# Kernel tuning notes

Measured on AMD Instinct MI355X. Metric: run time of the kernel, lower is better.

## Reference

```python
import jax, jax.numpy as jnp
import numpy as np

B, S, D, H, DFF = 2, 2048, 1024, 16, 4096
DK = D // H
EPS = 1e-05


def setup_inputs() -> dict:
    key = jax.random.key(0)
    ks = jax.random.split(key, 10)
    s = 0.02
    return {
        "x": jax.random.normal(ks[0], (B, S, D), jnp.float32),
        "src_mask": jnp.ones((B, 1, 1, S), jnp.int32),
        "wq": jax.random.normal(ks[1], (D, D), jnp.float32) * s,
        "wk": jax.random.normal(ks[2], (D, D), jnp.float32) * s,
        "wv": jax.random.normal(ks[3], (D, D), jnp.float32) * s,
        "wo": jax.random.normal(ks[4], (D, D), jnp.float32) * s,
        "w1": jax.random.normal(ks[5], (D, DFF), jnp.float32) * s,
        "b1": jnp.zeros((DFF,), jnp.float32),
        "w2": jax.random.normal(ks[6], (DFF, D), jnp.float32) * s,
        "b2": jnp.zeros((D,), jnp.float32),
        "gamma1": jnp.ones((), jnp.float32),
        "beta1": jnp.ones((), jnp.float32),
        "gamma2": jnp.ones((), jnp.float32),
        "beta2": jnp.ones((), jnp.float32),
    }


def layer_norm(x, gamma, beta):
    # torch.var uses unbiased estimator (ddof=1); gamma/beta are scalars
    mean = jnp.mean(x, axis=-1, keepdims=True)
    var = jnp.var(x, axis=-1, keepdims=True, ddof=1)
    return (x - mean) * gamma / jnp.sqrt(var + EPS) + beta


def mha(x, wq, wk, wv, wo):
    # Note: source's masked_fill is non-in-place with discarded result -> mask has no effect.
    q = (x @ wq).reshape(B, S, H, DK).transpose(0, 2, 1, 3)
    k = (x @ wk).reshape(B, S, H, DK).transpose(0, 2, 1, 3)
    v = (x @ wv).reshape(B, S, H, DK).transpose(0, 2, 1, 3)
    scores = jnp.einsum('bhqd,bhkd->bhqk', q, k) / jnp.sqrt(jnp.float32(DK))
    attn = jax.nn.softmax(scores, axis=-1)
    out = jnp.einsum('bhqk,bhkd->bhqd', attn, v)
    out = out.transpose(0, 2, 1, 3).reshape(B, S, D)
    return out @ wo


def reference(x, src_mask, wq, wk, wv, wo, w1, b1, w2, b2,
              gamma1, beta1, gamma2, beta2):
    # residual 1: attention (dropout = identity in eval)
    x = layer_norm(x + mha(x, wq, wk, wv, wo), gamma1, beta1)
    # residual 2: FFN
    ff = jax.nn.relu(x @ w1 + b1) @ w2 + b2
    x = layer_norm(x + ff, gamma2, beta2)
    return x
```

## Files before the change

### kernel.cpp

```cpp
#include <hip/hip_runtime.h>
#include <cstdio>

constexpr int B_   = 2;
constexpr int S_   = 2048;
constexpr int D_   = 1024;
constexpr int H_   = 16;
constexpr int DFF_ = 4096;
constexpr int DK_  = D_ / H_;
constexpr int M_   = B_ * S_;
constexpr float EPS_ = 1e-5f;
constexpr size_t MEGE = 1u << 20;
constexpr size_t QKV_STRIDE = 4 * MEGE;

typedef __attribute__((ext_vector_type(8))) short bf16x8;
typedef __attribute__((ext_vector_type(4))) float f32x4;

__device__ __forceinline__ float bf2f(unsigned int u) {
    return __uint_as_float(u << 16);
}
__device__ __forceinline__ unsigned short f2bf(float f) {
    unsigned int u = __float_as_uint(f);
    unsigned int r = u + 0x7fffu + ((u >> 16) & 1u);
    return (unsigned short)(r >> 16);
}
__device__ __forceinline__ unsigned short f2bf_rz(float f) {
    return (unsigned short)(__float_as_uint(f) >> 16);
}

__device__ __forceinline__ void gload_lds16(const unsigned short* g, unsigned short* l) {
    __builtin_amdgcn_global_load_lds(
        (const __attribute__((address_space(1))) unsigned int*)g,
        (__attribute__((address_space(3))) unsigned int*)l, 16, 0, 0);
}

__device__ __forceinline__ void tr32(const float* __restrict__ W, unsigned short* __restrict__ Wt,
                                     int K, int N, int bx, int by, float* t )
{
    const int tx = threadIdx.x & 31, ty = threadIdx.x >> 5;
    const int n0 = bx * 32, k0 = by * 32;
    #pragma unroll
    for (int p = 0; p < 4; ++p)
        t[(ty + p * 8) * 33 + tx] = W[(size_t)(k0 + ty + p * 8) * N + n0 + tx];
    __syncthreads();
    #pragma unroll
    for (int p = 0; p < 4; ++p)
        Wt[(size_t)(n0 + ty + p * 8) * K + k0 + tx] = f2bf(t[tx * 33 + ty + p * 8]);
}

__global__ __launch_bounds__(256)
void prep_k(const float* __restrict__ wq, const float* __restrict__ wk,
            const float* __restrict__ wv, const float* __restrict__ wo,
            const float* __restrict__ w1, const float* __restrict__ w2,
            const float* __restrict__ x,
            unsigned short* __restrict__ wqt, unsigned short* __restrict__ wkt,
            unsigned short* __restrict__ wvt, unsigned short* __restrict__ wot,
            unsigned short* __restrict__ w1t, unsigned short* __restrict__ w2t,
            unsigned short* __restrict__ xb)
{
    __shared__ float t[32 * 33];
    const int bid = blockIdx.x;
    if (bid < 4096) {
        const int z = bid >> 10, rem = bid & 1023;
        const float* W = (z == 0) ? wq : (z == 1) ? wk : (z == 2) ? wv : wo;
        unsigned short* Wt = (z == 0) ? wqt : (z == 1) ? wkt : (z == 2) ? wvt : wot;
        tr32(W, Wt, D_, D_, rem & 31, rem >> 5, t);
    } else if (bid < 8192) {
        const int rem = bid - 4096;
        tr32(w1, w1t, D_, DFF_, rem & 127, rem >> 7, t);
    } else if (bid < 12288) {
        const int rem = bid - 8192;
        tr32(w2, w2t, DFF_, D_, rem & 31, rem >> 5, t);
    } else {
        const int i = (bid - 12288) * 256 + threadIdx.x;
        float4 f = reinterpret_cast<const float4*>(x)[i];
        ushort4 u;
        u.x = f2bf(f.x); u.y = f2bf(f.y); u.z = f2bf(f.z); u.w = f2bf(f.w);
        reinterpret_cast<ushort4*>(xb)[i] = u;
    }
}

template<int BM, int OMODE, bool RELU>
__global__ __launch_bounds__(512, 2)
void mg2_k(const unsigned short* __restrict__ A,
           const unsigned short* __restrict__ Bt,
           const float* __restrict__ bias,
           unsigned short* __restrict__ C,
           int M, int N, int K, int Kld)
{
    constexpr int MI  = BM / 64;
    constexpr int AMH = (BM == 128) ? 2 : 1;
    __shared__ __align__(16) unsigned short As[2][BM * 64];
    __shared__ __align__(16) unsigned short Bs[2][256 * 64];

    const int z = blockIdx.z;
    A  += (size_t)z * K;
    Bt += (size_t)z * K;
    C  += (size_t)z * ((size_t)M * N);

    const int tid  = threadIdx.x;
    const int w    = tid >> 6, lane = tid & 63;
    const int l15  = lane & 15, quad = lane >> 4;
    const int wm   = w >> 2, wn = w & 3;
    const int m0   = blockIdx.y * BM, n0 = blockIdx.x * 256;
    const int NT   = K >> 6;

    const int srow = lane >> 3;
    const int schk = (lane & 7) ^ srow;
    const int rsw  = l15 & 7;

    f32x4 acc[2][MI][2][2];
    #pragma unroll
    for (int mh = 0; mh < 2; ++mh)
        #pragma unroll
        for (int mi = 0; mi < MI; ++mi)
            #pragma unroll
            for (int nh = 0; nh < 2; ++nh)
                #pragma unroll
                for (int nj = 0; nj < 2; ++nj)
                    acc[mh][mi][nh][nj] = (f32x4){0.f, 0.f, 0.f, 0.f};

    bf16x8 aA[AMH][MI][2];
    bf16x8 b0[2][2], b1[2][2];

    auto stage = [&](int tile, int type) {
        if (tile >= NT) return;
        const int buf = tile & 1;
        unsigned short* dst; const unsigned short* src; int r0;
        if (BM == 256) {
            if      (type == 0) { dst = &As[buf][0];        src = A;  r0 = m0; }
            else if (type == 1) { dst = &Bs[buf][0];        src = Bt; r0 = n0; }
            else if (type == 2) { dst = &Bs[buf][128 * 64]; src = Bt; r0 = n0 + 128; }
            else                { dst = &As[buf][128 * 64]; src = A;  r0 = m0 + 128; }
        } else {
            if      (type == 0) { dst = &Bs[buf][0];        src = Bt; r0 = n0; }
            else if (type == 1) { dst = &As[buf][0];        src = A;  r0 = m0; }
            else                { dst = &Bs[buf][128 * 64]; src = Bt; r0 = n0 + 128; }
        }
        const int k0 = tile * 64;
        #pragma unroll
        for (int g = 0; g < 2; ++g) {
            const int r = w * 16 + g * 8 + srow;
            gload_lds16(src + (size_t)(r0 + r) * Kld + k0 + schk * 8,
                        dst + (w * 16 + g * 8) * 64);
        }
    };
    auto rdA = [&](int buf, int mh, int amh) {
        const unsigned short* base = &As[buf][(BM == 256 && mh) ? 128 * 64 : 0];
        #pragma unroll
        for (int mi = 0; mi < MI; ++mi) {
            const int row = (BM == 256) ? (wm * 64 + mi * 16 + l15)
                                        : (wm * 64 + mh * 32 + mi * 16 + l15);
            const unsigned short* rp = base + row * 64;
            aA[amh][mi][0] = *reinterpret_cast<const bf16x8*>(rp + ((quad    ) ^ rsw) * 8);
            aA[amh][mi][1] = *reinterpret_cast<const bf16x8*>(rp + ((quad + 4) ^ rsw) * 8);
        }
    };
    auto rdB = [&](int buf, int nh, bf16x8 (&b)[2][2]) {
        const unsigned short* base = &Bs[buf][nh ? 128 * 64 : 0];
        #pragma unroll
        for (int nj = 0; nj < 2; ++nj) {
            const int row = wn * 32 + nj * 16 + l15;
            const unsigned short* rp = base + row * 64;
            b[nj][0] = *reinterpret_cast<const bf16x8*>(rp + ((quad    ) ^ rsw) * 8);
            b[nj][1] = *reinterpret_cast<const bf16x8*>(rp + ((quad + 4) ^ rsw) * 8);
        }
    };
    auto mm = [&](int mh, int amh, int nh, bf16x8 (&b)[2][2]) {
        __builtin_amdgcn_s_setprio(1);
        #pragma unroll
        for (int mi = 0; mi < MI; ++mi)
            #pragma unroll
            for (int nj = 0; nj < 2; ++nj) {
                acc[mh][mi][nh][nj] = __builtin_amdgcn_mfma_f32_16x16x32_bf16(
                    aA[amh][mi][0], b[nj][0], acc[mh][mi][nh][nj], 0, 0, 0);
                acc[mh][mi][nh][nj] = __builtin_amdgcn_mfma_f32_16x16x32_bf16(
                    aA[amh][mi][1], b[nj][1], acc[mh][mi][nh][nj], 0, 0, 0);
            }
        __builtin_amdgcn_s_setprio(0);
    };

    if (BM == 256) {
        stage(0, 0); stage(0, 1); stage(0, 2); stage(0, 3);
        stage(1, 0); stage(1, 1); stage(1, 2);
    } else {
        stage(0, 0); stage(0, 1); stage(0, 2);
        stage(1, 0); stage(1, 1);
    }

    for (int t = 0; t < NT; ++t) {
        const int cur = t & 1;
        if (t == NT - 1)    asm volatile("s_waitcnt vmcnt(0)" ::: "memory");
        else if (BM == 256) asm volatile("s_waitcnt vmcnt(6)" ::: "memory");
        else                asm volatile("s_waitcnt vmcnt(4)" ::: "memory");
        __builtin_amdgcn_s_barrier();

        if (BM == 256) {
            rdA(cur, 0, 0); rdB(cur, 0, b0); stage(t + 1, 3);
            __builtin_amdgcn_s_barrier();
            asm volatile("s_waitcnt lgkmcnt(0)" ::: "memory");
            mm(0, 0, 0, b0);
            __builtin_amdgcn_s_barrier();
            rdB(cur, 1, b1); stage(t + 2, 0);
            __builtin_amdgcn_s_barrier();
            asm volatile("s_waitcnt lgkmcnt(0)" ::: "memory");
            mm(0, 0, 1, b1);
            __builtin_amdgcn_s_barrier();
            rdA(cur, 1, 0); stage(t + 2, 1);
            __builtin_amdgcn_s_barrier();
            asm volatile("s_waitcnt lgkmcnt(0)" ::: "memory");
            mm(1, 0, 0, b0);
            __builtin_amdgcn_s_barrier();
            stage(t + 2, 2);
            __builtin_amdgcn_s_barrier();
            asm volatile("s_waitcnt lgkmcnt(0)" ::: "memory");
            mm(1, 0, 1, b1);
        } else {
            rdA(cur, 0, 0); rdA(cur, 1, 1); rdB(cur, 0, b0); stage(t + 1, 2);
            __builtin_amdgcn_s_barrier();
            asm volatile("s_waitcnt lgkmcnt(0)" ::: "memory");
            mm(0, 0, 0, b0); mm(1, 1, 0, b0);
            __builtin_amdgcn_s_barrier();
            rdB(cur, 1, b1); stage(t + 2, 0); stage(t + 2, 1);
            __builtin_amdgcn_s_barrier();
            asm volatile("s_waitcnt lgkmcnt(0)" ::: "memory");
            mm(0, 0, 1, b1); mm(1, 1, 1, b1);
        }
    }

    #pragma unroll
    for (int mh = 0; mh < 2; ++mh)
        #pragma unroll
        for (int mi = 0; mi < MI; ++mi) {
            const int mrow = (BM == 256) ? (mh * 128 + wm * 64 + mi * 16)
                                         : (wm * 64 + mh * 32 + mi * 16);
            #pragma unroll
            for (int r = 0; r < 4; ++r) {
                const int m = m0 + mrow + quad * 4 + r;
                #pragma unroll
                for (int nh = 0; nh < 2; ++nh)
                    #pragma unroll
                    for (int nj = 0; nj < 2; ++nj) {
                        const int n = n0 + nh * 128 + wn * 32 + nj * 16 + l15;
                        float v = acc[mh][mi][nh][nj][r];
                        if (bias) v += bias[n];
                        if (RELU) v = fmaxf(v, 0.0f);
                        size_t o;
                        if (OMODE == 2) {
                            int mat = n >> 10, nn = n & 1023;
                            int b = m >> 11, s = m & 2047;
                            int h = nn >> 6, dk = nn & 63;
                            o = (size_t)mat * QKV_STRIDE + (((size_t)b * H_ + h) * S_ + s) * DK_ + dk;
                        } else {
                            o = (size_t)m * N + n;
                        }
                        C[o] = f2bf(v);
                    }
            }
        }
}

__device__ __forceinline__ float wave_sum(float v) {
    #pragma unroll
    for (int off = 32; off > 0; off >>= 1) v += __shfl_down(v, off, 64);
    return v;
}

constexpr int TQ_ = 128;
constexpr int TK_ = 64;
constexpr int NT_ = S_ / TK_;

__global__ __launch_bounds__(256)
void fattn_k(const unsigned short* __restrict__ Qm, const unsigned short* __restrict__ Km,
             const unsigned short* __restrict__ Vm, unsigned short* __restrict__ O)
{
    const int bh  = blockIdx.x >> 4;
    const int qt  = blockIdx.x & 15;
    const int tid = threadIdx.x;
    const int w = tid >> 6, lane = tid & 63;
    const int quad = lane >> 4, l15 = lane & 15;
    const int sw = l15 & 7;

    __shared__ __align__(16) unsigned short Ks[2][TK_][64];
    __shared__ __align__(16) unsigned short Vt[2][80][64];
    __shared__ __align__(16) unsigned short Ps[4][32][64];

    bf16x8 qf[2][2];
    #pragma unroll
    for (int i = 0; i < 2; ++i) {
        const unsigned short* qp = Qm + ((size_t)bh * S_ + qt * TQ_ + w * 32 + i * 16 + l15) * DK_;
        qf[i][0] = *reinterpret_cast<const bf16x8*>(qp + quad * 8);
        qf[i][1] = *reinterpret_cast<const bf16x8*>(qp + 32 + quad * 8);
    }

    f32x4 o[2][4];
    f32x4 o4[2];
    #pragma unroll
    for (int i = 0; i < 2; ++i) {
        #pragma unroll
        for (int n = 0; n < 4; ++n) o[i][n] = (f32x4){0.f, 0.f, 0.f, 0.f};
        o4[i] = (f32x4){0.f, 0.f, 0.f, 0.f};
    }

    const unsigned short* kg0 = Km + (size_t)bh * S_ * DK_;
    const unsigned short* vg0 = Vm + (size_t)bh * S_ * DK_;
    const int dgrp = tid >> 4;
    const int vkp  = tid & 15;
    const int srow = lane >> 3;
    const int schk = (lane & 7) ^ srow;

    auto stageK = [&](int t, int buf) {
        const unsigned short* src = kg0 + (size_t)t * TK_ * DK_;
        #pragma unroll
        for (int g = 0; g < 2; ++g) {
            const int r0 = w * 16 + g * 8;
            gload_lds16(src + (size_t)(r0 + srow) * DK_ + schk * 8, &Ks[buf][r0][0]);
        }
    };
    auto loadV = [&](int t, ushort4 (&vp)[4]) {
        const unsigned short* vg = vg0 + (size_t)t * TK_ * DK_;
        #pragma unroll
        for (int p = 0; p < 4; ++p)
            vp[p] = reinterpret_cast<const ushort4*>(vg + (size_t)(vkp + p * 16) * DK_)[dgrp];
    };
    auto storeVt = [&](int buf, ushort4 (&vp)[4]) {
        char* base = reinterpret_cast<char*>(&Vt[buf][dgrp * 4][0]);
        const int cs = vkp >> 1, ch = (vkp & 1) << 3;
        ushort4 pk;
        pk.x = vp[0].x; pk.y = vp[1].x; pk.z = vp[2].x; pk.w = vp[3].x;
        *reinterpret_cast<ushort4*>(base + 0 * 128 + (((cs ^ ((dgrp * 4 + 0) & 7)) << 4) + ch)) = pk;
        pk.x = vp[0].y; pk.y = vp[1].y; pk.z = vp[2].y; pk.w = vp[3].y;
        *reinterpret_cast<ushort4*>(base + 1 * 128 + (((cs ^ ((dgrp * 4 + 1) & 7)) << 4) + ch)) = pk;
        pk.x = vp[0].z; pk.y = vp[1].z; pk.z = vp[2].z; pk.w = vp[3].z;
        *reinterpret_cast<ushort4*>(base + 2 * 128 + (((cs ^ ((dgrp * 4 + 2) & 7)) << 4) + ch)) = pk;
        pk.x = vp[0].w; pk.y = vp[1].w; pk.z = vp[2].w; pk.w = vp[3].w;
        *reinterpret_cast<ushort4*>(base + 3 * 128 + (((cs ^ ((dgrp * 4 + 3) & 7)) << 4) + ch)) = pk;
    };

    stageK(0, 0);
    {
        ushort4 vp0[4];
        loadV(0, vp0);
        storeVt(0, vp0);
        for (int idx = tid; idx < 2 * 16 * 64; idx += 256) {
            const int b  = idx >> 10;
            const int rr = (idx >> 6) & 15;
            const int cc = idx & 63;
            Vt[b][64 + rr][((cc >> 3) ^ (rr & 7)) * 8 + (cc & 7)] =
                (rr == 0) ? (unsigned short)0x3F80 : (unsigned short)0;
        }
    }

    for (int t = 0; t < NT_; ++t) {
        const int cur = t & 1, nxt = cur ^ 1;
        __syncthreads();

        const bool hn = (t + 1 < NT_);
        ushort4 vp[4];
        if (hn) { stageK(t + 1, nxt); loadV(t + 1, vp); }

        f32x4 s[2][4];
        __builtin_amdgcn_s_setprio(1);
        #pragma unroll
        for (int n = 0; n < 4; ++n) {
            const unsigned short* kp = &Ks[cur][n * 16 + l15][0];
            bf16x8 b0 = *reinterpret_cast<const bf16x8*>(kp + ((quad ^ sw) << 3));
            bf16x8 b1 = *reinterpret_cast<const bf16x8*>(kp + (((quad + 4) ^ sw) << 3));
            #pragma unroll
            for (int i = 0; i < 2; ++i) {
                f32x4 a2 = (f32x4){0.f, 0.f, 0.f, 0.f};
                a2 = __builtin_amdgcn_mfma_f32_16x16x32_bf16(qf[i][0], b0, a2, 0, 0, 0);
                a2 = __builtin_amdgcn_mfma_f32_16x16x32_bf16(qf[i][1], b1, a2, 0, 0, 0);
                s[i][n] = a2;
            }
        }
        __builtin_amdgcn_s_setprio(0);

        #pragma unroll
        for (int i = 0; i < 2; ++i)
            #pragma unroll
            for (int r = 0; r < 4; ++r) {
                ushort4 pk;
                pk.x = f2bf_rz(__expf(s[i][0][r] * 0.125f));
                pk.y = f2bf_rz(__expf(s[i][1][r] * 0.125f));
                pk.z = f2bf_rz(__expf(s[i][2][r] * 0.125f));
                pk.w = f2bf_rz(__expf(s[i][3][r] * 0.125f));
                const int R = i * 16 + quad * 4 + r;
                *reinterpret_cast<ushort4*>(
                    reinterpret_cast<char*>(&Ps[w][R][0]) +
                    ((((l15 >> 1) ^ (R & 7)) << 4) + ((l15 & 1) << 3))) = pk;
            }

        if (hn) storeVt(nxt, vp);

        bf16x8 pa[2][2];
        #pragma unroll
        for (int i = 0; i < 2; ++i) {
            const unsigned short* pp = &Ps[w][i * 16 + l15][0];
            pa[i][0] = *reinterpret_cast<const bf16x8*>(pp + ((quad ^ sw) << 3));
            pa[i][1] = *reinterpret_cast<const bf16x8*>(pp + (((quad + 4) ^ sw) << 3));
        }
        __builtin_amdgcn_s_setprio(1);
        #pragma unroll
        for (int n = 0; n < 4; ++n) {
            const unsigned short* vb = &Vt[cur][n * 16 + l15][0];
            bf16x8 vb0 = *reinterpret_cast<const bf16x8*>(vb + ((quad ^ sw) << 3));
            bf16x8 vb1 = *reinterpret_cast<const bf16x8*>(vb + (((quad + 4) ^ sw) << 3));
            #pragma unroll
            for (int i = 0; i < 2; ++i) {
                o[i][n] = __builtin_amdgcn_mfma_f32_16x16x32_bf16(pa[i][0], vb0, o[i][n], 0, 0, 0);
                o[i][n] = __builtin_amdgcn_mfma_f32_16x16x32_bf16(pa[i][1], vb1, o[i][n], 0, 0, 0);
            }
        }
        {
            const unsigned short* vb = &Vt[cur][64 + l15][0];
            bf16x8 vb40 = *reinterpret_cast<const bf16x8*>(vb + ((quad ^ sw) << 3));
            bf16x8 vb41 = *reinterpret_cast<const bf16x8*>(vb + (((quad + 4) ^ sw) << 3));
            #pragma unroll
            for (int i = 0; i < 2; ++i) {
                o4[i] = __builtin_amdgcn_mfma_f32_16x16x32_bf16(pa[i][0], vb40, o4[i], 0, 0, 0);
                o4[i] = __builtin_amdgcn_mfma_f32_16x16x32_bf16(pa[i][1], vb41, o4[i], 0, 0, 0);
            }
        }
        __builtin_amdgcn_s_setprio(0);
    }

    const int b = bh >> 4, h = bh & 15;
    #pragma unroll
    for (int i = 0; i < 2; ++i)
        #pragma unroll
        for (int r = 0; r < 4; ++r) {
            float lrv = __shfl(o4[i][r], lane & 0x30, 64);
            float inv = 1.0f / lrv;
            int q = qt * TQ_ + w * 32 + i * 16 + quad * 4 + r;
            unsigned short* op = O + ((size_t)b * S_ + q) * D_ + h * DK_;
            #pragma unroll
            for (int n = 0; n < 4; ++n)
                op[n * 16 + l15] = f2bf(o[i][n][r] * inv);
        }
}

template<bool HAS_BIAS, bool RES_F32, bool OUT_F32>
__global__ __launch_bounds__(256)
void lnr_k(const unsigned short* __restrict__ P0, const unsigned short* __restrict__ P1,
           const void* __restrict__ res, const float* __restrict__ bias,
           const float* __restrict__ gp, const float* __restrict__ bp,
           void* __restrict__ Out)
{
    const int row = blockIdx.x;
    const int tid = threadIdx.x;
    const int lane = tid & 63, wave = tid >> 6;
    __shared__ float rs[4], rss[4];

    const size_t i4 = (size_t)row * 256 + tid;
    const ushort4 a = reinterpret_cast<const ushort4*>(P0)[i4];
    const ushort4 b = reinterpret_cast<const ushort4*>(P1)[i4];
    float v0 = bf2f(a.x) + bf2f(b.x);
    float v1 = bf2f(a.y) + bf2f(b.y);
    float v2 = bf2f(a.z) + bf2f(b.z);
    float v3 = bf2f(a.w) + bf2f(b.w);
    if (RES_F32) {
        float4 rv = reinterpret_cast<const float4*>(res)[i4];
        v0 += rv.x; v1 += rv.y; v2 += rv.z; v3 += rv.w;
    } else {
        ushort4 rv = reinterpret_cast<const ushort4*>(res)[i4];
        v0 += bf2f(rv.x); v1 += bf2f(rv.y); v2 += bf2f(rv.z); v3 += bf2f(rv.w);
    }
    if (HAS_BIAS) {
        float4 bv = reinterpret_cast<const float4*>(bias)[tid];
        v0 += bv.x; v1 += bv.y; v2 += bv.z; v3 += bv.w;
    }

    float s  = v0 + v1 + v2 + v3;
    float ss = v0*v0 + v1*v1 + v2*v2 + v3*v3;
    s = wave_sum(s);
    ss = wave_sum(ss);
    if (lane == 0) { rs[wave] = s; rss[wave] = ss; }
    __syncthreads();
    const float stot  = rs[0] + rs[1] + rs[2] + rs[3];
    const float sstot = rss[0] + rss[1] + rss[2] + rss[3];
    const float mean = stot / (float)D_;
    const float var  = (sstot - (float)D_ * mean * mean) / (float)(D_ - 1);
    const float scl = gp[0] * rsqrtf(var + EPS_);
    const float be = bp[0];

    float o0 = (v0 - mean) * scl + be;
    float o1 = (v1 - mean) * scl + be;
    float o2 = (v2 - mean) * scl + be;
    float o3 = (v3 - mean) * scl + be;
    if (OUT_F32) {
        reinterpret_cast<float4*>(Out)[i4] = make_float4(o0, o1, o2, o3);
    } else {
        ushort4 o;
        o.x = f2bf(o0); o.y = f2bf(o1); o.z = f2bf(o2); o.w = f2bf(o3);
        reinterpret_cast<ushort4*>(Out)[i4] = o;
    }
}

extern "C" void kernel_launch(void* const* d_in, const int* in_sizes, int n_in,
                              void* d_out, int out_size, void* d_ws, size_t ws_size,
                              hipStream_t stream)
{
    const float* x   = (const float*)d_in[0];
    const float* wq  = (const float*)d_in[2];
    const float* wk  = (const float*)d_in[3];
    const float* wv  = (const float*)d_in[4];
    const float* wo  = (const float*)d_in[5];
    const float* w1  = (const float*)d_in[6];
    const float* b1  = (const float*)d_in[7];
    const float* w2  = (const float*)d_in[8];
    const float* b2  = (const float*)d_in[9];
    const float* g1  = (const float*)d_in[10];
    const float* be1 = (const float*)d_in[11];
    const float* g2  = (const float*)d_in[12];
    const float* be2 = (const float*)d_in[13];

    unsigned short* ws = (unsigned short*)d_ws;
    const size_t need_bytes = 32 * MEGE * 2;
    if (ws_size < need_bytes) {
        fprintf(stderr, "kernel_launch: ws too small (%zu < %zu)\n", ws_size, need_bytes);
    }
    unsigned short* wqt = ws + 0 * MEGE;
    unsigned short* wkt = ws + 1 * MEGE;
    unsigned short* wvt = ws + 2 * MEGE;
    unsigned short* wot = ws + 3 * MEGE;
    unsigned short* w1t = ws + 4 * MEGE;
    unsigned short* w2t = ws + 8 * MEGE;
    unsigned short* xb  = ws + 12 * MEGE;
    unsigned short* Q   = ws + 16 * MEGE;
    unsigned short* K   = ws + 20 * MEGE;
    unsigned short* V   = ws + 24 * MEGE;
    unsigned short* AO  = ws + 28 * MEGE;
    unsigned short* x1  = xb;
    unsigned short* WP  = ws + 16 * MEGE;
    unsigned short* h1  = ws + 16 * MEGE;
    unsigned short* FP  = ws + 0 * MEGE;

    prep_k<<<dim3(16384), 256, 0, stream>>>(wq, wk, wv, wo, w1, w2, x,
                                            wqt, wkt, wvt, wot, w1t, w2t, xb);

    mg2_k<256, 2, false><<<dim3(3 * D_ / 256, M_ / 256), 512, 0, stream>>>(
        xb, wqt, nullptr, Q, M_, 3 * D_, D_, D_);

    fattn_k<<<dim3(B_ * H_ * (S_ / TQ_)), 256, 0, stream>>>(Q, K, V, AO);

    mg2_k<128, 0, false><<<dim3(D_ / 256, M_ / 128, 2), 512, 0, stream>>>(
        AO, wot, nullptr, WP, M_, D_, D_ / 2, D_);

    lnr_k<false, true, false><<<dim3(M_), 256, 0, stream>>>(
        WP, WP + 4 * MEGE, x, nullptr, g1, be1, x1);

    mg2_k<256, 0, true><<<dim3(DFF_ / 256, M_ / 256), 512, 0, stream>>>(
        x1, w1t, b1, h1, M_, DFF_, D_, D_);

    mg2_k<128, 0, false><<<dim3(D_ / 256, M_ / 128, 2), 512, 0, stream>>>(
        h1, w2t, nullptr, FP, M_, D_, DFF_ / 2, DFF_);

    lnr_k<true, false, true><<<dim3(M_), 256, 0, stream>>>(
        FP, FP + 4 * MEGE, x1, b2, g2, be2, d_out);
}
```

Baseline: 342.3 us.

## Split attention tile across 8 waves and fold softmax scale into Q projection

The flash-attention kernel now launches 512 threads, so each of eight waves handles 16 query rows instead of 32, and K staging and V loading are divided between the two halves of the block. The 1/sqrt(dk)·log2(e) factor is folded into Q inside the QKV GEMM epilogue, which lets the softmax use a raw v_exp_f32 (exp2) with no per-element multiply. The aim is more waves to hide latency and fewer VALU ops per score. In exchange each wave gets less MFMA reuse per K/V LDS read, and rounding Q after scaling slightly changes numerics.

Measured after the change: 325.7 us. 4.8% less time.

```diff
diff --git a/kernel.cpp b/kernel.cpp
--- a/kernel.cpp
+++ b/kernel.cpp
@@ -11,6 +11,7 @@
 constexpr float EPS_ = 1e-5f;
 constexpr size_t MEGE = 1u << 20;
 constexpr size_t QKV_STRIDE = 4 * MEGE;
+constexpr float QSCALE_ = 0.18033688011112042f;
 
 typedef __attribute__((ext_vector_type(8))) short bf16x8;
 typedef __attribute__((ext_vector_type(4))) float f32x4;
@@ -25,6 +26,11 @@
 }
 __device__ __forceinline__ unsigned short f2bf_rz(float f) {
     return (unsigned short)(__float_as_uint(f) >> 16);
+}
+__device__ __forceinline__ float exp2_fast(float x) {
+    float r;
+    asm("v_exp_f32 %0, %1" : "=v"(r) : "v"(x));
+    return r;
 }
 
 __device__ __forceinline__ void gload_lds16(const unsigned short* g, unsigned short* l) {
@@ -249,6 +255,7 @@
                             int mat = n >> 10, nn = n & 1023;
                             int b = m >> 11, s = m & 2047;
                             int h = nn >> 6, dk = nn & 63;
+                            if (mat == 0) v *= QSCALE_;
                             o = (size_t)mat * QKV_STRIDE + (((size_t)b * H_ + h) * S_ + s) * DK_ + dk;
                         } else {
                             o = (size_t)m * N + n;
@@ -269,7 +276,7 @@
 constexpr int TK_ = 64;
 constexpr int NT_ = S_ / TK_;
 
-__global__ __launch_bounds__(256)
+__global__ __launch_bounds__(512)
 void fattn_k(const unsigned short* __restrict__ Qm, const unsigned short* __restrict__ Km,
              const unsigned short* __restrict__ Vm, unsigned short* __restrict__ O)
 {
@@ -282,24 +289,20 @@
 
     __shared__ __align__(16) unsigned short Ks[2][TK_][64];
     __shared__ __align__(16) unsigned short Vt[2][80][64];
-    __shared__ __align__(16) unsigned short Ps[4][32][64];
-
-    bf16x8 qf[2][2];
-    #pragma unroll
-    for (int i = 0; i < 2; ++i) {
-        const unsigned short* qp = Qm + ((size_t)bh * S_ + qt * TQ_ + w * 32 + i * 16 + l15) * DK_;
-        qf[i][0] = *reinterpret_cast<const bf16x8*>(qp + quad * 8);
-        qf[i][1] = *reinterpret_cast<const bf16x8*>(qp + 32 + quad * 8);
-    }
-
-    f32x4 o[2][4];
-    f32x4 o4[2];
-    #pragma unroll
-    for (int i = 0; i < 2; ++i) {
-        #pragma unroll
-        for (int n = 0; n < 4; ++n) o[i][n] = (f32x4){0.f, 0.f, 0.f, 0.f};
-        o4[i] = (f32x4){0.f, 0.f, 0.f, 0.f};
-    }
+    __shared__ __align__(16) unsigned short Ps[8][16][64];
+
+    bf16x8 qf0, qf1;
+    {
+        const unsigned short* qp = Qm + ((size_t)bh * S_ + qt * TQ_ + w * 16 + l15) * DK_;
+        qf0 = *reinterpret_cast<const bf16x8*>(qp + quad * 8);
+        qf1 = *reinterpret_cast<const bf16x8*>(qp + 32 + quad * 8);
+    }
+
+    f32x4 o[4];
+    f32x4 o4;
+    #pragma unroll
+    for (int n = 0; n < 4; ++n) o[n] = (f32x4){0.f, 0.f, 0.f, 0.f};
+    o4 = (f32x4){0.f, 0.f, 0.f, 0.f};
 
     const unsigned short* kg0 = Km + (size_t)bh * S_ * DK_;
     const unsigned short* vg0 = Vm + (size_t)bh * S_ * DK_;
@@ -310,9 +313,10 @@
 
     auto stageK = [&](int t, int buf) {
         const unsigned short* src = kg0 + (size_t)t * TK_ * DK_;
+        const int wk = w - 4;
         #pragma unroll
         for (int g = 0; g < 2; ++g) {
-            const int r0 = w * 16 + g * 8;
+            const int r0 = wk * 16 + g * 8;
             gload_lds16(src + (size_t)(r0 + srow) * DK_ + schk * 8, &Ks[buf][r0][0]);
         }
     };
@@ -336,18 +340,18 @@
         *reinterpret_cast<ushort4*>(base + 3 * 128 + (((cs ^ ((dgrp * 4 + 3) & 7)) << 4) + ch)) = pk;
     };
 
-    stageK(0, 0);
-    {
+    if (w >= 4) stageK(0, 0);
+    else {
         ushort4 vp0[4];
         loadV(0, vp0);
         storeVt(0, vp0);
-        for (int idx = tid; idx < 2 * 16 * 64; idx += 256) {
-            const int b  = idx >> 10;
-            const int rr = (idx >> 6) & 15;
-            const int cc = idx & 63;
-            Vt[b][64 + rr][((cc >> 3) ^ (rr & 7)) * 8 + (cc & 7)] =
-                (rr == 0) ? (unsigned short)0x3F80 : (unsigned short)0;
-        }
+    }
+    for (int idx = tid; idx < 2 * 16 * 64; idx += 512) {
+        const int b  = idx >> 10;
+        const int rr = (idx >> 6) & 15;
+        const int cc = idx & 63;
+        Vt[b][64 + rr][((cc >> 3) ^ (rr & 7)) * 8 + (cc & 7)] =
+            (rr == 0) ? (unsigned short)0x3F80 : (unsigned short)0;
     }
 
     for (int t = 0; t < NT_; ++t) {
@@ -356,48 +360,42 @@
 
         const bool hn = (t + 1 < NT_);
         ushort4 vp[4];
-        if (hn) { stageK(t + 1, nxt); loadV(t + 1, vp); }
-
-        f32x4 s[2][4];
+        if (hn) { if (w >= 4) stageK(t + 1, nxt); else loadV(t + 1, vp); }
+
+        f32x4 s[4];
         __builtin_amdgcn_s_setprio(1);
         #pragma unroll
         for (int n = 0; n < 4; ++n) {
             const unsigned short* kp = &Ks[cur][n * 16 + l15][0];
             bf16x8 b0 = *reinterpret_cast<const bf16x8*>(kp + ((quad ^ sw) << 3));
             bf16x8 b1 = *reinterpret_cast<const bf16x8*>(kp + (((quad + 4) ^ sw) << 3));
-            #pragma unroll
-            for (int i = 0; i < 2; ++i) {
-                f32x4 a2 = (f32x4){0.f, 0.f, 0.f, 0.f};
-                a2 = __builtin_amdgcn_mfma_f32_16x16x32_bf16(qf[i][0], b0, a2, 0, 0, 0);
-                a2 = __builtin_amdgcn_mfma_f32_16x16x32_bf16(qf[i][1], b1, a2, 0, 0, 0);
-                s[i][n] = a2;
-            }
+            f32x4 a2 = (f32x4){0.f, 0.f, 0.f, 0.f};
+            a2 = __builtin_amdgcn_mfma_f32_16x16x32_bf16(qf0, b0, a2, 0, 0, 0);
+            a2 = __builtin_amdgcn_mfma_f32_16x16x32_bf16(qf1, b1, a2, 0, 0, 0);
+            s[n] = a2;
         }
         __builtin_amdgcn_s_setprio(0);
 
         #pragma unroll
-        for (int i = 0; i < 2; ++i)
-            #pragma unroll
-            for (int r = 0; r < 4; ++r) {
-                ushort4 pk;
-                pk.x = f2bf_rz(__expf(s[i][0][r] * 0.125f));
-                pk.y = f2bf_rz(__expf(s[i][1][r] * 0.125f));
-                pk.z = f2bf_rz(__expf(s[i][2][r] * 0.125f));
-                pk.w = f2bf_rz(__expf(s[i][3][r] * 0.125f));
-                const int R = i * 16 + quad * 4 + r;
-                *reinterpret_cast<ushort4*>(
-                    reinterpret_cast<char*>(&Ps[w][R][0]) +
-                    ((((l15 >> 1) ^ (R & 7)) << 4) + ((l15 & 1) << 3))) = pk;
-            }
-
-        if (hn) storeVt(nxt, vp);
-
-        bf16x8 pa[2][2];
-        #pragma unroll
-        for (int i = 0; i < 2; ++i) {
-            const unsigned short* pp = &Ps[w][i * 16 + l15][0];
-            pa[i][0] = *reinterpret_cast<const bf16x8*>(pp + ((quad ^ sw) << 3));
-            pa[i][1] = *reinterpret_cast<const bf16x8*>(pp + (((quad + 4) ^ sw) << 3));
+        for (int r = 0; r < 4; ++r) {
+            ushort4 pk;
+            pk.x = f2bf_rz(exp2_fast(s[0][r]));
+            pk.y = f2bf_rz(exp2_fast(s[1][r]));
+            pk.z = f2bf_rz(exp2_fast(s[2][r]));
+            pk.w = f2bf_rz(exp2_fast(s[3][r]));
+            const int R = quad * 4 + r;
+            *reinterpret_cast<ushort4*>(
+                reinterpret_cast<char*>(&Ps[w][R][0]) +
+                ((((l15 >> 1) ^ (R & 7)) << 4) + ((l15 & 1) << 3))) = pk;
+        }
+
+        if (hn && w < 4) storeVt(nxt, vp);
+
+        bf16x8 pa0, pa1;
+        {
+            const unsigned short* pp = &Ps[w][l15][0];
+            pa0 = *reinterpret_cast<const bf16x8*>(pp + ((quad ^ sw) << 3));
+            pa1 = *reinterpret_cast<const bf16x8*>(pp + (((quad + 4) ^ sw) << 3));
         }
         __builtin_amdgcn_s_setprio(1);
         #pragma unroll
@@ -405,38 +403,30 @@
             const unsigned short* vb = &Vt[cur][n * 16 + l15][0];
             bf16x8 vb0 = *reinterpret_cast<const bf16x8*>(vb + ((quad ^ sw) << 3));
             bf16x8 vb1 = *reinterpret_cast<const bf16x8*>(vb + (((quad + 4) ^ sw) << 3));
-            #pragma unroll
-            for (int i = 0; i < 2; ++i) {
-                o[i][n] = __builtin_amdgcn_mfma_f32_16x16x32_bf16(pa[i][0], vb0, o[i][n], 0, 0, 0);
-                o[i][n] = __builtin_amdgcn_mfma_f32_16x16x32_bf16(pa[i][1], vb1, o[i][n], 0, 0, 0);
-            }
+            o[n] = __builtin_amdgcn_mfma_f32_16x16x32_bf16(pa0, vb0, o[n], 0, 0, 0);
+            o[n] = __builtin_amdgcn_mfma_f32_16x16x32_bf16(pa1, vb1, o[n], 0, 0, 0);
         }
         {
             const unsigned short* vb = &Vt[cur][64 + l15][0];
             bf16x8 vb40 = *reinterpret_cast<const bf16x8*>(vb + ((quad ^ sw) << 3));
             bf16x8 vb41 = *reinterpret_cast<const bf16x8*>(vb + (((quad + 4) ^ sw) << 3));
-            #pragma unroll
-            for (int i = 0; i < 2; ++i) {
-                o4[i] = __builtin_amdgcn_mfma_f32_16x16x32_bf16(pa[i][0], vb40, o4[i], 0, 0, 0);
-                o4[i] = __builtin_amdgcn_mfma_f32_16x16x32_bf16(pa[i][1], vb41, o4[i], 0, 0, 0);
-            }
+            o4 = __builtin_amdgcn_mfma_f32_16x16x32_bf16(pa0, vb40, o4, 0, 0, 0);
+            o4 = __builtin_amdgcn_mfma_f32_16x16x32_bf16(pa1, vb41, o4, 0, 0, 0);
         }
         __builtin_amdgcn_s_setprio(0);
     }
 
     const int b = bh >> 4, h = bh & 15;
     #pragma unroll
-    for (int i = 0; i < 2; ++i)
-        #pragma unroll
-        for (int r = 0; r < 4; ++r) {
-            float lrv = __shfl(o4[i][r], lane & 0x30, 64);
-            float inv = 1.0f / lrv;
-            int q = qt * TQ_ + w * 32 + i * 16 + quad * 4 + r;
-            unsigned short* op = O + ((size_t)b * S_ + q) * D_ + h * DK_;
-            #pragma unroll
-            for (int n = 0; n < 4; ++n)
-                op[n * 16 + l15] = f2bf(o[i][n][r] * inv);
-        }
+    for (int r = 0; r < 4; ++r) {
+        float lrv = __shfl(o4[r], lane & 0x30, 64);
+        float inv = 1.0f / lrv;
+        int q = qt * TQ_ + w * 16 + quad * 4 + r;
+        unsigned short* op = O + ((size_t)b * S_ + q) * D_ + h * DK_;
+        #pragma unroll
+        for (int n = 0; n < 4; ++n)
+            op[n * 16 + l15] = f2bf(o[n][r] * inv);
+    }
 }
 
 template<bool HAS_BIAS, bool RES_F32, bool OUT_F32>
@@ -541,7 +531,7 @@
     mg2_k<256, 2, false><<<dim3(3 * D_ / 256, M_ / 256), 512, 0, stream>>>(
         xb, wqt, nullptr, Q, M_, 3 * D_, D_, D_);
 
-    fattn_k<<<dim3(B_ * H_ * (S_ / TQ_)), 256, 0, stream>>>(Q, K, V, AO);
+    fattn_k<<<dim3(B_ * H_ * (S_ / TQ_)), 512, 0, stream>>>(Q, K, V, AO);
 
     mg2_k<128, 0, false><<<dim3(D_ / 256, M_ / 128, 2), 512, 0, stream>>>(
         AO, wot, nullptr, WP, M_, D_, D_ / 2, D_);
```
